# Optimization experiments

Measured on AMD Instinct MI355X. Metric: run time of the kernel, lower is better.

The kernel has to match this reference:

```python
import math
import jax, jax.numpy as jnp
import numpy as np

EPS = 1e-6
MAX_SCALE_LOG = math.log(100.0)

def rms_norm(x, scale, eps=EPS):
    # x * scale / rms(x), reduction over last dim
    ms = jnp.mean(jnp.square(x), axis=-1, keepdims=True)
    return x * (scale * jax.lax.rsqrt(ms + eps))

def axial_rope_theta(pos, n_heads, d_head, dtype):
    # freqs: linspace in log-space from pi to 10*pi, reshaped to [n_heads, d_head//4]
    f = np.exp(np.linspace(math.log(math.pi), math.log(10.0 * math.pi),
                           n_heads * d_head // 4 + 1)[:-1])
    freqs = jnp.asarray(f.reshape(d_head // 4, n_heads).T, dtype)  # [h, e/4]
    theta_h = pos[:, :, None, 0:1] * freqs  # [n, l, h, e/4]
    theta_w = pos[:, :, None, 1:2] * freqs  # [n, l, h, e/4]
    theta = jnp.concatenate([theta_h, theta_w], axis=-1)  # [n, l, h, e/2]
    return theta.transpose(0, 2, 1, 3)  # [n, h, l, e/2]

def apply_rotary(x, theta):
    d = theta.shape[-1]
    x1, x2, x3 = x[..., :d], x[..., d:2 * d], x[..., 2 * d:]
    cos, sin = jnp.cos(theta), jnp.sin(theta)
    return jnp.concatenate([x1 * cos - x2 * sin, x2 * cos + x1 * sin, x3], axis=-1)

def setup_inputs() -> dict:
    key = jax.random.key(0)
    ks = jax.random.split(key, 8)
    n, l, d_model, d_head = 2, 2048, 1024, 64
    n_heads = d_model // d_head
    x = jax.random.normal(ks[0], (n, l, d_model), jnp.float32)
    pos = jax.random.uniform(ks[1], (n, l, 2), jnp.float32)
    cond = jax.random.normal(ks[2], (n, 1, d_model), jnp.float32)
    # params (torch uses zero-init for w_cond/w_out; small random for a non-degenerate baseline)
    w_cond = jax.random.normal(ks[3], (d_model, d_model), jnp.float32) * 0.02
    w_qkv = jax.random.normal(ks[4], (d_model, 3 * d_model), jnp.float32) * (d_model ** -0.5)
    qk_scale = jnp.full((n_heads,), math.log(10.0), jnp.float32)
    w_out = jax.random.normal(ks[5], (d_model, d_model), jnp.float32) * 0.02
    return {"x": x, "pos": pos, "cond": cond, "w_cond": w_cond,
            "w_qkv": w_qkv, "qk_scale": qk_scale, "w_out": w_out}

def reference(x, pos, cond, w_cond, w_qkv, qk_scale, w_out):
    n, l, d_model = x.shape
    h = qk_scale.shape[0]
    e = d_model // h
    # AdaRMSNorm: scale = linear(cond) + 1
    xn = rms_norm(x, cond @ w_cond + 1.0)
    # QKV projection
    q, k, v = jnp.split(xn @ w_qkv, 3, axis=-1)
    to_heads = lambda t: t.reshape(n, l, h, e).transpose(0, 2, 1, 3)  # [n,h,l,e]
    q, k, v = to_heads(q), to_heads(k), to_heads(v)
    # QKNorm: per-head learned scale, rms over head dim
    s = jnp.exp(0.5 * jnp.minimum(qk_scale, MAX_SCALE_LOG) - 0.25 * math.log(e))
    q = rms_norm(q, s[:, None, None])
    k = rms_norm(k, s[:, None, None])
    # Axial RoPE
    theta = axial_rope_theta(pos, h, e, x.dtype)
    q = apply_rotary(q, theta)
    k = apply_rotary(k, theta)
    # SDPA (no mask)
    attn = jax.nn.softmax(jnp.einsum('nhqe,nhke->nhqk', q, k) / math.sqrt(e), axis=-1)
    o = jnp.einsum('nhqk,nhke->nhqe', attn, v)
    o = o.transpose(0, 2, 1, 3).reshape(n, l, d_model)
    return o @ w_out
```

## Files before the change

### kernel.cpp

```cpp
#include <hip/hip_runtime.h>

typedef unsigned short u16;
typedef unsigned int u32;
typedef short s16x8 __attribute__((ext_vector_type(8)));
typedef short s16x4 __attribute__((ext_vector_type(4)));
typedef float f32x4 __attribute__((ext_vector_type(4)));
typedef u32 u32x2 __attribute__((ext_vector_type(2)));

#define AS1 __attribute__((address_space(1)))
#define AS3 __attribute__((address_space(3)))

__device__ __forceinline__ float bf2f(u16 u) {
    union { unsigned int i; float f; } x; x.i = ((unsigned int)u) << 16; return x.f;
}
__device__ __forceinline__ u16 f2bf(float f) {
    union { float f; unsigned int i; } x; x.f = f;
    unsigned int r = (x.i + 0x7FFFu + ((x.i >> 16) & 1u)) >> 16;
    return (u16)r;
}
__device__ __forceinline__ void storeOut(u16* p, float v) { *p = f2bf(v); }
__device__ __forceinline__ void storeOut(float* p, float v) { *p = v; }
__device__ __forceinline__ float loadIn(const void* p, size_t i, int isf32) {
    return isf32 ? ((const float*)p)[i] : bf2f(((const u16*)p)[i]);
}
__device__ __forceinline__ float fexp2(float x) {
#if __has_builtin(__builtin_amdgcn_exp2f)
    return __builtin_amdgcn_exp2f(x);
#else
    return exp2f(x);
#endif
}
__device__ __forceinline__ u32 pack_bf(float a, float b) {
    u32 ua = __float_as_uint(a) + 0x8000u;
    u32 ub = __float_as_uint(b) + 0x8000u;
    return __builtin_amdgcn_perm(ub, ua, 0x07060302u);
}

__global__ __launch_bounds__(256) void detect_dtype(const u16* __restrict__ x,
                                                    int* __restrict__ flag) {
    __shared__ int cnt[4];
    const int tid = threadIdx.x;
    int c = 0;
    #pragma unroll
    for (int i = 0; i < 4; ++i) {
        const u16 u = x[tid * 4 + i];
        const int e = (u >> 7) & 0xFF;
        c += (e >= 101 && e <= 135) ? 1 : 0;
    }
    #pragma unroll
    for (int m = 1; m < 64; m <<= 1) c += __shfl_xor(c, m, 64);
    if ((tid & 63) == 0) cnt[tid >> 6] = c;
    __syncthreads();
    if (tid == 0) {
        const int t = cnt[0] + cnt[1] + cnt[2] + cnt[3];
        *flag = (t < 800) ? 1 : 0;
    }
}

__global__ __launch_bounds__(256) void cond_gemv(const void* __restrict__ cond,
                                                 const void* __restrict__ w,
                                                 float* __restrict__ out,
                                                 const int* __restrict__ flag) {
    const int isf32 = *flag;
    const int d  = blockIdx.x * 256 + threadIdx.x;
    const int n  = blockIdx.y;
    const int k0 = blockIdx.z * 64;
    float acc = 0.f;
    #pragma unroll 8
    for (int k = 0; k < 64; ++k)
        acc += loadIn(cond, n * 1024 + k0 + k, isf32) *
               loadIn(w, (size_t)(k0 + k) * 1024 + d, isf32);
    atomicAdd(out + n * 1024 + d, acc);
}

__global__ __launch_bounds__(256) void rmsnorm_x(const void* __restrict__ x,
                                                 const float* __restrict__ scl,
                                                 u16* __restrict__ xn,
                                                 const int* __restrict__ flag) {
    const int isf32 = *flag;
    const int tok = blockIdx.x;
    const int n = tok >> 11;
    u16* orow = xn + (size_t)tok * 1024;
    const int base = threadIdx.x * 4;
    float f0, f1, f2, f3;
    if (isf32) {
        const float4 v = *(const float4*)((const float*)x + (size_t)tok * 1024 + base);
        f0 = v.x; f1 = v.y; f2 = v.z; f3 = v.w;
    } else {
        s16x4 uv = *(const s16x4*)((const u16*)x + (size_t)tok * 1024 + base);
        f0 = bf2f((u16)uv[0]); f1 = bf2f((u16)uv[1]); f2 = bf2f((u16)uv[2]); f3 = bf2f((u16)uv[3]);
    }
    float ss = f0 * f0 + f1 * f1 + f2 * f2 + f3 * f3;
    #pragma unroll
    for (int m = 1; m < 64; m <<= 1) ss += __shfl_xor(ss, m, 64);
    __shared__ float red[4];
    const int wave = threadIdx.x >> 6, lane = threadIdx.x & 63;
    if (lane == 0) red[wave] = ss;
    __syncthreads();
    float ms = (red[0] + red[1] + red[2] + red[3]) * (1.f / 1024.f);
    float rinv = rsqrtf(ms + 1e-6f);
    orow[base + 0] = f2bf(f0 * (scl[n * 1024 + base + 0] + 1.f) * rinv);
    orow[base + 1] = f2bf(f1 * (scl[n * 1024 + base + 1] + 1.f) * rinv);
    orow[base + 2] = f2bf(f2 * (scl[n * 1024 + base + 2] + 1.f) * rinv);
    orow[base + 3] = f2bf(f3 * (scl[n * 1024 + base + 3] + 1.f) * rinv);
}

__global__ __launch_bounds__(256) void transpose_bf(const void* __restrict__ src,
                                                    u16* __restrict__ dst, int R, int C,
                                                    const int* __restrict__ flag) {
    const int isf32 = *flag;
    __shared__ u16 t[32][33];
    const int c0 = blockIdx.x * 32, r0 = blockIdx.y * 32;
    const int tx = threadIdx.x & 31, ty = threadIdx.x >> 5;
    #pragma unroll
    for (int i = 0; i < 4; ++i)
        t[ty + i * 8][tx] = f2bf(loadIn(src, (size_t)(r0 + ty + i * 8) * C + c0 + tx, isf32));
    __syncthreads();
    #pragma unroll
    for (int i = 0; i < 4; ++i)
        dst[(size_t)(c0 + ty + i * 8) * R + r0 + tx] = t[tx][ty + i * 8];
}

template <typename OutT>
__global__ __launch_bounds__(256) void gemm_bt(const u16* __restrict__ A,
                                               const u16* __restrict__ BT,
                                               OutT* __restrict__ C, int Nn, int K) {
    __shared__ u16 As[128 * 32];
    __shared__ u16 Bs[128 * 32];
    const int tid = threadIdx.x;
    const int wave = tid >> 6, lane = tid & 63;
    const int l15 = lane & 15, quad = lane >> 4;
    const int bm0 = blockIdx.y * 128, bn0 = blockIdx.x * 128;
    const int wr = wave >> 1, wc = wave & 1;
    f32x4 acc[4][4] = {};
    const int srow = lane >> 2;
    const int g = (lane & 3) ^ (srow & 3);
    for (int bk = 0; bk < K; bk += 32) {
        __syncthreads();
        #pragma unroll
        for (int p = 0; p < 2; ++p) {
            const int rowl = p * 64 + wave * 16 + srow;
            __builtin_amdgcn_global_load_lds(
                (const AS1 void*)(A + (size_t)(bm0 + rowl) * K + bk + g * 8),
                (AS3 void*)(As + (p * 64 + wave * 16) * 32), 16, 0, 0);
            __builtin_amdgcn_global_load_lds(
                (const AS1 void*)(BT + (size_t)(bn0 + rowl) * K + bk + g * 8),
                (AS3 void*)(Bs + (p * 64 + wave * 16) * 32), 16, 0, 0);
        }
        __syncthreads();
        s16x8 af[4], bfr[4];
        #pragma unroll
        for (int mt = 0; mt < 4; ++mt) {
            const int r = wr * 64 + mt * 16 + l15;
            af[mt] = *(const s16x8*)(As + r * 32 + ((quad ^ (r & 3)) << 3));
        }
        #pragma unroll
        for (int nt = 0; nt < 4; ++nt) {
            const int r = wc * 64 + nt * 16 + l15;
            bfr[nt] = *(const s16x8*)(Bs + r * 32 + ((quad ^ (r & 3)) << 3));
        }
        #pragma unroll
        for (int mt = 0; mt < 4; ++mt)
            #pragma unroll
            for (int nt = 0; nt < 4; ++nt)
                acc[mt][nt] = __builtin_amdgcn_mfma_f32_16x16x32_bf16(af[mt], bfr[nt], acc[mt][nt], 0, 0, 0);
    }
    #pragma unroll
    for (int mt = 0; mt < 4; ++mt)
        #pragma unroll
        for (int nt = 0; nt < 4; ++nt)
            #pragma unroll
            for (int r = 0; r < 4; ++r) {
                const int row = bm0 + wr * 64 + mt * 16 + quad * 4 + r;
                const int col = bn0 + wc * 64 + nt * 16 + l15;
                storeOut(C + (size_t)row * Nn + col, acc[mt][nt][r]);
            }
}

__global__ __launch_bounds__(256) void qkv_head(const u16* __restrict__ qkv,
                                                const void* __restrict__ pos,
                                                const void* __restrict__ qk_scale,
                                                u16* __restrict__ q_ws,
                                                u16* __restrict__ k_ws,
                                                u16* __restrict__ vtg,
                                                const int* __restrict__ flag) {
    const int isf32 = *flag;
    const int nh = blockIdx.y;
    const int n = nh >> 4, h = nh & 15;
    const int l0 = blockIdx.x * 64;
    const int tid = threadIdx.x;
    const int wave = tid >> 6, lane = tid & 63;

    const float qs = loadIn(qk_scale, h, isf32);
    const float s = __expf(0.5f * fminf(qs, 4.605170186f) - 1.039720771f);
    const float qmul = s * s * 0.125f * 1.44269504089f;
    const int j = lane & 31;
    const float t = (float)((j & 15) * 16 + h);
    const float freq = 3.14159265358979f * __expf(t * (2.302585093f / 256.f));
    const int pj = j >> 4;

    #pragma unroll 2
    for (int it = 0; it < 16; ++it) {
        const int l = l0 + wave * 16 + it;
        const int tok = n * 2048 + l;
        const u16* row = qkv + (size_t)tok * 3072;
        float qv = bf2f(row[h * 64 + lane]);
        float kv = bf2f(row[1024 + h * 64 + lane]);
        float q2 = qv * qv, k2 = kv * kv;
        #pragma unroll
        for (int m = 1; m < 64; m <<= 1) { q2 += __shfl_xor(q2, m, 64); k2 += __shfl_xor(k2, m, 64); }
        float qn = qv * rsqrtf(q2 * (1.f / 64.f) + 1e-6f) * qmul;
        float kn = kv * rsqrtf(k2 * (1.f / 64.f) + 1e-6f);
        const float p = loadIn(pos, tok * 2 + pj, isf32);
        const float th = p * freq;
        const float c = __cosf(th), sn = __sinf(th);
        const float pq = __shfl_xor(qn, 32, 64);
        const float pk = __shfl_xor(kn, 32, 64);
        float qr, kr;
        if (lane < 32) { qr = qn * c - pq * sn; kr = kn * c - pk * sn; }
        else           { qr = qn * c + pq * sn; kr = kn * c + pk * sn; }
        const size_t oidx = ((size_t)nh * 2048 + l) * 64 + lane;
        q_ws[oidx] = f2bf(qr);
        k_ws[oidx] = f2bf(kr);
    }

    __shared__ u16 tbuf[64][65];
    const u16* vsrc = qkv + (size_t)(n * 2048 + l0) * 3072 + 2048 + h * 64;
    #pragma unroll
    for (int it = 0; it < 16; ++it) {
        const int idx = it * 256 + tid;
        const int r = idx >> 6, c = idx & 63;
        tbuf[r][c] = vsrc[(size_t)r * 3072 + c];
    }
    __syncthreads();
    u16* dst = vtg + (size_t)nh * 131072 + l0;
    #pragma unroll
    for (int it = 0; it < 16; ++it) {
        const int idx = it * 256 + tid;
        const int er = idx >> 6, lc = idx & 63;
        dst[(size_t)er * 2048 + lc] = tbuf[lc][er];
    }
}

__global__ __launch_bounds__(256, 2) void attn7(const u16* __restrict__ Q,
                                                const u16* __restrict__ K,
                                                const u16* __restrict__ Vtg,
                                                float* __restrict__ Opart,
                                                float* __restrict__ lpart) {
    __shared__ u16 Ks[2][64 * 64];
    __shared__ u16 Vt[2][64 * 64];
    __shared__ u16 Ps[4][64 * 72];
    const int nh = blockIdx.y;
    const int q0 = blockIdx.x * 256;
    const int ks = blockIdx.z;
    const int kb0 = ks * 1024;
    const int tid = threadIdx.x;
    const int wave = tid >> 6, lane = tid & 63;
    const int l15 = lane & 15, quad = lane >> 4;
    const size_t hb = (size_t)nh * 2048 * 64;
    const u16* Vbase = Vtg + (size_t)nh * 131072;
    const int dr0 = tid >> 3;
    const int dd  = tid & 7;

    s16x8 qf[4][2];
    #pragma unroll
    for (int qg = 0; qg < 4; ++qg)
        #pragma unroll
        for (int kc = 0; kc < 2; ++kc)
            qf[qg][kc] = *(const s16x8*)(Q + hb + (size_t)(q0 + wave * 64 + qg * 16 + l15) * 64 + kc * 32 + quad * 8);

    f32x4 Oacc[4][4] = {};
    float lacc[4] = {0.f, 0.f, 0.f, 0.f};
    u16* Pw = Ps[wave];

    #pragma unroll
    for (int it = 0; it < 2; ++it) {
        const int row = it * 32 + dr0;
        const int g = dd ^ (row & 7);
        __builtin_amdgcn_global_load_lds(
            (const AS1 void*)(K + hb + (size_t)(kb0 + row) * 64 + g * 8),
            (AS3 void*)(Ks[0] + (it * 256 + wave * 64) * 8), 16, 0, 0);
        __builtin_amdgcn_global_load_lds(
            (const AS1 void*)(Vbase + (size_t)row * 2048 + kb0 + g * 8),
            (AS3 void*)(Vt[0] + (it * 256 + wave * 64) * 8), 16, 0, 0);
    }
    __syncthreads();

    for (int i = 0; i < 16; ++i) {
        const int cur = i & 1;
        const int kb = kb0 + i * 64;
        if (i < 15) {
            const int nxt = cur ^ 1;
            const int kbn = kb + 64;
            #pragma unroll
            for (int it = 0; it < 2; ++it) {
                const int row = it * 32 + dr0;
                const int g = dd ^ (row & 7);
                __builtin_amdgcn_global_load_lds(
                    (const AS1 void*)(K + hb + (size_t)(kbn + row) * 64 + g * 8),
                    (AS3 void*)(Ks[nxt] + (it * 256 + wave * 64) * 8), 16, 0, 0);
                __builtin_amdgcn_global_load_lds(
                    (const AS1 void*)(Vbase + (size_t)row * 2048 + kbn + g * 8),
                    (AS3 void*)(Vt[nxt] + (it * 256 + wave * 64) * 8), 16, 0, 0);
            }
        }

        f32x4 S[4][4];
        #pragma unroll
        for (int qg = 0; qg < 4; ++qg)
            #pragma unroll
            for (int kt = 0; kt < 4; ++kt) {
                S[qg][kt][0] = -15.f; S[qg][kt][1] = -15.f;
                S[qg][kt][2] = -15.f; S[qg][kt][3] = -15.f;
            }
        #pragma unroll
        for (int kt = 0; kt < 4; ++kt) {
            const int r = kt * 16 + l15;
            #pragma unroll
            for (int kc = 0; kc < 2; ++kc) {
                const s16x8 kf = *(const s16x8*)(Ks[cur] + r * 64 + (((kc * 4 + quad) ^ (r & 7)) << 3));
                #pragma unroll
                for (int qg = 0; qg < 4; ++qg)
                    S[qg][kt] = __builtin_amdgcn_mfma_f32_16x16x32_bf16(kf, qf[qg][kc], S[qg][kt], 0, 0, 0);
            }
        }

        #pragma unroll
        for (int qg = 0; qg < 4; ++qg) {
            float rs = 0.f;
            #pragma unroll
            for (int kt = 0; kt < 4; ++kt) {
                const float e0 = fexp2(S[qg][kt][0]);
                const float e1 = fexp2(S[qg][kt][1]);
                const float e2 = fexp2(S[qg][kt][2]);
                const float e3 = fexp2(S[qg][kt][3]);
                rs += (e0 + e1) + (e2 + e3);
                u32x2 pk2;
                pk2[0] = pack_bf(e0, e1);
                pk2[1] = pack_bf(e2, e3);
                *(u32x2*)(Pw + (qg * 16 + l15) * 72 + kt * 16 + quad * 4) = pk2;
            }
            lacc[qg] += rs;
        }

        #pragma unroll
        for (int kc = 0; kc < 2; ++kc) {
            s16x8 pf[4];
            #pragma unroll
            for (int qg = 0; qg < 4; ++qg)
                pf[qg] = *(const s16x8*)(Pw + (qg * 16 + l15) * 72 + kc * 32 + quad * 8);
            #pragma unroll
            for (int nto = 0; nto < 4; ++nto) {
                const int e = nto * 16 + l15;
                const s16x8 vf = *(const s16x8*)(Vt[cur] + e * 64 + (((kc * 4 + quad) ^ (e & 7)) << 3));
                #pragma unroll
                for (int qg = 0; qg < 4; ++qg)
                    Oacc[qg][nto] = __builtin_amdgcn_mfma_f32_16x16x32_bf16(pf[qg], vf, Oacc[qg][nto], 0, 0, 0);
            }
        }

        if (i < 15) __syncthreads();
    }

    #pragma unroll
    for (int qg = 0; qg < 4; ++qg) {
        lacc[qg] += __shfl_xor(lacc[qg], 16, 64);
        lacc[qg] += __shfl_xor(lacc[qg], 32, 64);
    }

    const size_t pb = ((size_t)(ks * 32 + nh)) * 2048;
    if (quad == 0) {
        #pragma unroll
        for (int qg = 0; qg < 4; ++qg)
            lpart[pb + q0 + wave * 64 + qg * 16 + l15] = lacc[qg];
    }
    #pragma unroll
    for (int qg = 0; qg < 4; ++qg)
        #pragma unroll
        for (int r = 0; r < 4; ++r) {
            const int qrow = q0 + wave * 64 + qg * 16 + quad * 4 + r;
            float* orow = Opart + (pb + qrow) * 64;
            #pragma unroll
            for (int nto = 0; nto < 4; ++nto)
                orow[nto * 16 + l15] = Oacc[qg][nto][r];
        }
}

__global__ __launch_bounds__(256) void combine_o(const float* __restrict__ Opart,
                                                 const float* __restrict__ lpart,
                                                 u16* __restrict__ O) {
    constexpr size_t HS = (size_t)32 * 2048 * 64;
    constexpr size_t LS = (size_t)32 * 2048;
    const int tok = blockIdx.x;
    const int n = tok >> 11, l = tok & 2047;
    const int idx = threadIdx.x * 4;
    const int h = idx >> 6;
    const int nh = n * 16 + h;
    const size_t base = ((size_t)nh * 2048 + l) * 64 + (idx & 63);
    const float4 a = *(const float4*)(Opart + base);
    const float4 b = *(const float4*)(Opart + HS + base);
    const float inv = 1.f / (lpart[(size_t)nh * 2048 + l] + lpart[LS + (size_t)nh * 2048 + l]);
    u16* o = O + (size_t)tok * 1024 + idx;
    o[0] = f2bf((a.x + b.x) * inv);
    o[1] = f2bf((a.y + b.y) * inv);
    o[2] = f2bf((a.z + b.z) * inv);
    o[3] = f2bf((a.w + b.w) * inv);
}

extern "C" void kernel_launch(void* const* d_in, const int* in_sizes, int n_in,
                              void* d_out, int out_size, void* d_ws, size_t ws_size,
                              hipStream_t stream) {
    const void* x        = d_in[0];
    const void* pos      = d_in[1];
    const void* cond     = d_in[2];
    const void* w_cond   = d_in[3];
    const void* w_qkv    = d_in[4];
    const void* qk_scale = d_in[5];
    const void* w_out    = d_in[6];

    char* ws = (char*)d_ws;
    constexpr size_t MB = 1048576;
    constexpr size_t OFS_SCALE = 0;
    constexpr size_t OFS_FLAG  = 8192;
    constexpr size_t OFS_WOUTT = 16384;
    constexpr size_t OFS_Q     = OFS_WOUTT + 2 * MB;
    constexpr size_t OFS_K     = OFS_Q     + 8 * MB;
    constexpr size_t OFS_VT    = OFS_K     + 8 * MB;
    constexpr size_t OFS_O     = OFS_VT    + 8 * MB;
    constexpr size_t OFS_XN    = OFS_O     + 8 * MB;
    constexpr size_t OFS_WQKVT = OFS_XN    + 8 * MB;
    constexpr size_t OFS_QKV   = OFS_WQKVT + 6 * MB;
    constexpr size_t OFS_OPART = OFS_XN;
    constexpr size_t OFS_LPART = OFS_OPART + 32 * MB;

    float* scale = (float*)(ws + OFS_SCALE);
    int*   flag  = (int*)(ws + OFS_FLAG);
    u16* xn    = (u16*)(ws + OFS_XN);
    u16* wqkvT = (u16*)(ws + OFS_WQKVT);
    u16* woutT = (u16*)(ws + OFS_WOUTT);
    u16* qkv   = (u16*)(ws + OFS_QKV);
    u16* qws   = (u16*)(ws + OFS_Q);
    u16* kws   = (u16*)(ws + OFS_K);
    u16* vtg   = (u16*)(ws + OFS_VT);
    u16* ows   = (u16*)(ws + OFS_O);
    float* opart = (float*)(ws + OFS_OPART);
    float* lpart = (float*)(ws + OFS_LPART);

    detect_dtype<<<dim3(1), 256, 0, stream>>>((const u16*)x, flag);
    hipMemsetAsync(scale, 0, 2 * 1024 * sizeof(float), stream);
    cond_gemv<<<dim3(4, 2, 16), 256, 0, stream>>>(cond, w_cond, scale, flag);
    rmsnorm_x<<<dim3(4096), 256, 0, stream>>>(x, scale, xn, flag);
    transpose_bf<<<dim3(96, 32), 256, 0, stream>>>(w_qkv, wqkvT, 1024, 3072, flag);
    transpose_bf<<<dim3(32, 32), 256, 0, stream>>>(w_out, woutT, 1024, 1024, flag);
    gemm_bt<u16><<<dim3(24, 32), 256, 0, stream>>>(xn, wqkvT, qkv, 3072, 1024);
    qkv_head<<<dim3(32, 32), 256, 0, stream>>>(qkv, pos, qk_scale, qws, kws, vtg, flag);
    attn7<<<dim3(8, 32, 2), 256, 0, stream>>>(qws, kws, vtg, opart, lpart);
    combine_o<<<dim3(4096), 256, 0, stream>>>(opart, lpart, ows);
    gemm_bt<float><<<dim3(8, 32), 256, 0, stream>>>(ows, woutT, (float*)d_out, 1024, 1024);
}
```

Baseline: 248.2 us.

## Double-buffer GEMM LDS tiles, inline dtype detection, merge weight transposes

Replaces the GEMM with a double-buffered LDS version that prefetches the next K tile while running MFMAs on the current one, leaving one barrier per iteration. The output projection moves to a 128x64 tile variant so it launches more blocks. The dtype-detection kernel is removed, and each kernel now recomputes the flag from the first 1024 elements of x within one wave. The two weight transposes are merged into a single launch. Together these aim to cut launch count and hide global-load latency, at the cost of extra LDS per block, redundant per-block detection loads, and idle early-exit blocks in the merged transpose.

Measured after the change: 242.8 us. 2.2% less time.

```diff
diff --git a/kernel.cpp b/kernel.cpp
--- a/kernel.cpp
+++ b/kernel.cpp
@@ -35,33 +35,25 @@
     u32 ub = __float_as_uint(b) + 0x8000u;
     return __builtin_amdgcn_perm(ub, ua, 0x07060302u);
 }
-
-__global__ __launch_bounds__(256) void detect_dtype(const u16* __restrict__ x,
-                                                    int* __restrict__ flag) {
-    __shared__ int cnt[4];
-    const int tid = threadIdx.x;
+__device__ __forceinline__ int detect_f32(const u16* __restrict__ x) {
+    const int lane = threadIdx.x & 63;
     int c = 0;
     #pragma unroll
-    for (int i = 0; i < 4; ++i) {
-        const u16 u = x[tid * 4 + i];
+    for (int i = 0; i < 16; ++i) {
+        const u16 u = x[lane * 16 + i];
         const int e = (u >> 7) & 0xFF;
         c += (e >= 101 && e <= 135) ? 1 : 0;
     }
     #pragma unroll
     for (int m = 1; m < 64; m <<= 1) c += __shfl_xor(c, m, 64);
-    if ((tid & 63) == 0) cnt[tid >> 6] = c;
-    __syncthreads();
-    if (tid == 0) {
-        const int t = cnt[0] + cnt[1] + cnt[2] + cnt[3];
-        *flag = (t < 800) ? 1 : 0;
-    }
+    return c < 800;
 }
 
 __global__ __launch_bounds__(256) void cond_gemv(const void* __restrict__ cond,
                                                  const void* __restrict__ w,
                                                  float* __restrict__ out,
-                                                 const int* __restrict__ flag) {
-    const int isf32 = *flag;
+                                                 const u16* __restrict__ xdet) {
+    const int isf32 = detect_f32(xdet);
     const int d  = blockIdx.x * 256 + threadIdx.x;
     const int n  = blockIdx.y;
     const int k0 = blockIdx.z * 64;
@@ -75,9 +67,8 @@
 
 __global__ __launch_bounds__(256) void rmsnorm_x(const void* __restrict__ x,
                                                  const float* __restrict__ scl,
-                                                 u16* __restrict__ xn,
-                                                 const int* __restrict__ flag) {
-    const int isf32 = *flag;
+                                                 u16* __restrict__ xn) {
+    const int isf32 = detect_f32((const u16*)x);
     const int tok = blockIdx.x;
     const int n = tok >> 11;
     u16* orow = xn + (size_t)tok * 1024;
@@ -105,10 +96,18 @@
     orow[base + 3] = f2bf(f3 * (scl[n * 1024 + base + 3] + 1.f) * rinv);
 }
 
-__global__ __launch_bounds__(256) void transpose_bf(const void* __restrict__ src,
-                                                    u16* __restrict__ dst, int R, int C,
-                                                    const int* __restrict__ flag) {
-    const int isf32 = *flag;
+__global__ __launch_bounds__(256) void transpose_w(const void* __restrict__ wqkv,
+                                                   const void* __restrict__ wout,
+                                                   u16* __restrict__ dqkv,
+                                                   u16* __restrict__ dout,
+                                                   const u16* __restrict__ xdet) {
+    const int z = blockIdx.z;
+    if (z == 1 && blockIdx.x >= 32) return;
+    const int isf32 = detect_f32(xdet);
+    const void* src = z ? wout : wqkv;
+    u16* dst = z ? dout : dqkv;
+    const int C = z ? 1024 : 3072;
+    const int R = 1024;
     __shared__ u16 t[32][33];
     const int c0 = blockIdx.x * 32, r0 = blockIdx.y * 32;
     const int tx = threadIdx.x & 31, ty = threadIdx.x >> 5;
@@ -122,11 +121,11 @@
 }
 
 template <typename OutT>
-__global__ __launch_bounds__(256) void gemm_bt(const u16* __restrict__ A,
-                                               const u16* __restrict__ BT,
-                                               OutT* __restrict__ C, int Nn, int K) {
-    __shared__ u16 As[128 * 32];
-    __shared__ u16 Bs[128 * 32];
+__global__ __launch_bounds__(256, 3) void gemm2(const u16* __restrict__ A,
+                                                const u16* __restrict__ BT,
+                                                OutT* __restrict__ C, int Nn, int K) {
+    __shared__ u16 As[2][128 * 32];
+    __shared__ u16 Bs[2][128 * 32];
     const int tid = threadIdx.x;
     const int wave = tid >> 6, lane = tid & 63;
     const int l15 = lane & 15, quad = lane >> 4;
@@ -135,35 +134,50 @@
     f32x4 acc[4][4] = {};
     const int srow = lane >> 2;
     const int g = (lane & 3) ^ (srow & 3);
-    for (int bk = 0; bk < K; bk += 32) {
-        __syncthreads();
-        #pragma unroll
-        for (int p = 0; p < 2; ++p) {
-            const int rowl = p * 64 + wave * 16 + srow;
-            __builtin_amdgcn_global_load_lds(
-                (const AS1 void*)(A + (size_t)(bm0 + rowl) * K + bk + g * 8),
-                (AS3 void*)(As + (p * 64 + wave * 16) * 32), 16, 0, 0);
-            __builtin_amdgcn_global_load_lds(
-                (const AS1 void*)(BT + (size_t)(bn0 + rowl) * K + bk + g * 8),
-                (AS3 void*)(Bs + (p * 64 + wave * 16) * 32), 16, 0, 0);
-        }
-        __syncthreads();
+    #pragma unroll
+    for (int p = 0; p < 2; ++p) {
+        const int rowl = p * 64 + wave * 16 + srow;
+        __builtin_amdgcn_global_load_lds(
+            (const AS1 void*)(A + (size_t)(bm0 + rowl) * K + g * 8),
+            (AS3 void*)(As[0] + (p * 64 + wave * 16) * 32), 16, 0, 0);
+        __builtin_amdgcn_global_load_lds(
+            (const AS1 void*)(BT + (size_t)(bn0 + rowl) * K + g * 8),
+            (AS3 void*)(Bs[0] + (p * 64 + wave * 16) * 32), 16, 0, 0);
+    }
+    __syncthreads();
+    const int iters = K >> 5;
+    for (int it = 0; it < iters; ++it) {
+        const int cur = it & 1;
+        if (it + 1 < iters) {
+            const int bkn = (it + 1) << 5;
+            #pragma unroll
+            for (int p = 0; p < 2; ++p) {
+                const int rowl = p * 64 + wave * 16 + srow;
+                __builtin_amdgcn_global_load_lds(
+                    (const AS1 void*)(A + (size_t)(bm0 + rowl) * K + bkn + g * 8),
+                    (AS3 void*)(As[cur ^ 1] + (p * 64 + wave * 16) * 32), 16, 0, 0);
+                __builtin_amdgcn_global_load_lds(
+                    (const AS1 void*)(BT + (size_t)(bn0 + rowl) * K + bkn + g * 8),
+                    (AS3 void*)(Bs[cur ^ 1] + (p * 64 + wave * 16) * 32), 16, 0, 0);
+            }
+        }
         s16x8 af[4], bfr[4];
         #pragma unroll
         for (int mt = 0; mt < 4; ++mt) {
             const int r = wr * 64 + mt * 16 + l15;
-            af[mt] = *(const s16x8*)(As + r * 32 + ((quad ^ (r & 3)) << 3));
+            af[mt] = *(const s16x8*)(As[cur] + r * 32 + ((quad ^ (r & 3)) << 3));
         }
         #pragma unroll
         for (int nt = 0; nt < 4; ++nt) {
             const int r = wc * 64 + nt * 16 + l15;
-            bfr[nt] = *(const s16x8*)(Bs + r * 32 + ((quad ^ (r & 3)) << 3));
+            bfr[nt] = *(const s16x8*)(Bs[cur] + r * 32 + ((quad ^ (r & 3)) << 3));
         }
         #pragma unroll
         for (int mt = 0; mt < 4; ++mt)
             #pragma unroll
             for (int nt = 0; nt < 4; ++nt)
                 acc[mt][nt] = __builtin_amdgcn_mfma_f32_16x16x32_bf16(af[mt], bfr[nt], acc[mt][nt], 0, 0, 0);
+        if (it + 1 < iters) __syncthreads();
     }
     #pragma unroll
     for (int mt = 0; mt < 4; ++mt)
@@ -173,6 +187,76 @@
             for (int r = 0; r < 4; ++r) {
                 const int row = bm0 + wr * 64 + mt * 16 + quad * 4 + r;
                 const int col = bn0 + wc * 64 + nt * 16 + l15;
+                storeOut(C + (size_t)row * Nn + col, acc[mt][nt][r]);
+            }
+}
+
+template <typename OutT>
+__global__ __launch_bounds__(256, 3) void gemm2_64(const u16* __restrict__ A,
+                                                   const u16* __restrict__ BT,
+                                                   OutT* __restrict__ C, int Nn, int K) {
+    __shared__ u16 As[2][128 * 32];
+    __shared__ u16 Bs[2][64 * 32];
+    const int tid = threadIdx.x;
+    const int wave = tid >> 6, lane = tid & 63;
+    const int l15 = lane & 15, quad = lane >> 4;
+    const int bm0 = blockIdx.y * 128, bn0 = blockIdx.x * 64;
+    f32x4 acc[2][4] = {};
+    const int srow = lane >> 2;
+    const int g = (lane & 3) ^ (srow & 3);
+    #pragma unroll
+    for (int p = 0; p < 2; ++p) {
+        const int rowl = p * 64 + wave * 16 + srow;
+        __builtin_amdgcn_global_load_lds(
+            (const AS1 void*)(A + (size_t)(bm0 + rowl) * K + g * 8),
+            (AS3 void*)(As[0] + (p * 64 + wave * 16) * 32), 16, 0, 0);
+    }
+    __builtin_amdgcn_global_load_lds(
+        (const AS1 void*)(BT + (size_t)(bn0 + wave * 16 + srow) * K + g * 8),
+        (AS3 void*)(Bs[0] + (wave * 16) * 32), 16, 0, 0);
+    __syncthreads();
+    const int iters = K >> 5;
+    for (int it = 0; it < iters; ++it) {
+        const int cur = it & 1;
+        if (it + 1 < iters) {
+            const int bkn = (it + 1) << 5;
+            #pragma unroll
+            for (int p = 0; p < 2; ++p) {
+                const int rowl = p * 64 + wave * 16 + srow;
+                __builtin_amdgcn_global_load_lds(
+                    (const AS1 void*)(A + (size_t)(bm0 + rowl) * K + bkn + g * 8),
+                    (AS3 void*)(As[cur ^ 1] + (p * 64 + wave * 16) * 32), 16, 0, 0);
+            }
+            __builtin_amdgcn_global_load_lds(
+                (const AS1 void*)(BT + (size_t)(bn0 + wave * 16 + srow) * K + bkn + g * 8),
+                (AS3 void*)(Bs[cur ^ 1] + (wave * 16) * 32), 16, 0, 0);
+        }
+        s16x8 af[2], bfr[4];
+        #pragma unroll
+        for (int mt = 0; mt < 2; ++mt) {
+            const int r = wave * 32 + mt * 16 + l15;
+            af[mt] = *(const s16x8*)(As[cur] + r * 32 + ((quad ^ (r & 3)) << 3));
+        }
+        #pragma unroll
+        for (int nt = 0; nt < 4; ++nt) {
+            const int r = nt * 16 + l15;
+            bfr[nt] = *(const s16x8*)(Bs[cur] + r * 32 + ((quad ^ (r & 3)) << 3));
+        }
+        #pragma unroll
+        for (int mt = 0; mt < 2; ++mt)
+            #pragma unroll
+            for (int nt = 0; nt < 4; ++nt)
+                acc[mt][nt] = __builtin_amdgcn_mfma_f32_16x16x32_bf16(af[mt], bfr[nt], acc[mt][nt], 0, 0, 0);
+        if (it + 1 < iters) __syncthreads();
+    }
+    #pragma unroll
+    for (int mt = 0; mt < 2; ++mt)
+        #pragma unroll
+        for (int nt = 0; nt < 4; ++nt)
+            #pragma unroll
+            for (int r = 0; r < 4; ++r) {
+                const int row = bm0 + wave * 32 + mt * 16 + quad * 4 + r;
+                const int col = bn0 + nt * 16 + l15;
                 storeOut(C + (size_t)row * Nn + col, acc[mt][nt][r]);
             }
 }
@@ -183,8 +267,8 @@
                                                 u16* __restrict__ q_ws,
                                                 u16* __restrict__ k_ws,
                                                 u16* __restrict__ vtg,
-                                                const int* __restrict__ flag) {
-    const int isf32 = *flag;
+                                                const u16* __restrict__ xdet) {
+    const int isf32 = detect_f32(xdet);
     const int nh = blockIdx.y;
     const int n = nh >> 4, h = nh & 15;
     const int l0 = blockIdx.x * 64;
@@ -417,11 +501,11 @@
     const void* w_qkv    = d_in[4];
     const void* qk_scale = d_in[5];
     const void* w_out    = d_in[6];
+    const u16* xdet = (const u16*)x;
 
     char* ws = (char*)d_ws;
     constexpr size_t MB = 1048576;
     constexpr size_t OFS_SCALE = 0;
-    constexpr size_t OFS_FLAG  = 8192;
     constexpr size_t OFS_WOUTT = 16384;
     constexpr size_t OFS_Q     = OFS_WOUTT + 2 * MB;
     constexpr size_t OFS_K     = OFS_Q     + 8 * MB;
@@ -434,7 +518,6 @@
     constexpr size_t OFS_LPART = OFS_OPART + 32 * MB;
 
     float* scale = (float*)(ws + OFS_SCALE);
-    int*   flag  = (int*)(ws + OFS_FLAG);
     u16* xn    = (u16*)(ws + OFS_XN);
     u16* wqkvT = (u16*)(ws + OFS_WQKVT);
     u16* woutT = (u16*)(ws + OFS_WOUTT);
@@ -446,15 +529,13 @@
     float* opart = (float*)(ws + OFS_OPART);
     float* lpart = (float*)(ws + OFS_LPART);
 
-    detect_dtype<<<dim3(1), 256, 0, stream>>>((const u16*)x, flag);
     hipMemsetAsync(scale, 0, 2 * 1024 * sizeof(float), stream);
-    cond_gemv<<<dim3(4, 2, 16), 256, 0, stream>>>(cond, w_cond, scale, flag);
-    rmsnorm_x<<<dim3(4096), 256, 0, stream>>>(x, scale, xn, flag);
-    transpose_bf<<<dim3(96, 32), 256, 0, stream>>>(w_qkv, wqkvT, 1024, 3072, flag);
-    transpose_bf<<<dim3(32, 32), 256, 0, stream>>>(w_out, woutT, 1024, 1024, flag);
-    gemm_bt<u16><<<dim3(24, 32), 256, 0, stream>>>(xn, wqkvT, qkv, 3072, 1024);
-    qkv_head<<<dim3(32, 32), 256, 0, stream>>>(qkv, pos, qk_scale, qws, kws, vtg, flag);
+    cond_gemv<<<dim3(4, 2, 16), 256, 0, stream>>>(cond, w_cond, scale, xdet);
+    rmsnorm_x<<<dim3(4096), 256, 0, stream>>>(x, scale, xn);
+    transpose_w<<<dim3(96, 32, 2), 256, 0, stream>>>(w_qkv, w_out, wqkvT, woutT, xdet);
+    gemm2<u16><<<dim3(24, 32), 256, 0, stream>>>(xn, wqkvT, qkv, 3072, 1024);
+    qkv_head<<<dim3(32, 32), 256, 0, stream>>>(qkv, pos, qk_scale, qws, kws, vtg, xdet);
     attn7<<<dim3(8, 32, 2), 256, 0, stream>>>(qws, kws, vtg, opart, lpart);
     combine_o<<<dim3(4096), 256, 0, stream>>>(opart, lpart, ows);
-    gemm_bt<float><<<dim3(8, 32), 256, 0, stream>>>(ows, woutT, (float*)d_out, 1024, 1024);
-}
+    gemm2_64<float><<<dim3(16, 32), 256, 0, stream>>>(ows, woutT, (float*)d_out, 1024, 1024);
+}
```
